# Kernel optimization log

Hardware: AMD Instinct MI355X
Metric: run time of the kernel (lower is better)

Reference implementation:

```python
import jax, jax.numpy as jnp
import numpy as np

B, S, H, W, C = 1, 14, 56, 56, 192
WS = 7            # cubic window
SH = 3            # shift
HEADS = 6
HD = C // HEADS
N = WS ** 3       # 343 tokens per window
NW = (S // WS) * (H // WS) * (W // WS)  # 128 windows
SCALE = HD ** -0.5
HID = 4 * C
TBL = (2 * WS - 1) ** 3  # 2197


def _rel_index():
    # faithful to torch: meshgrid with indexing='xy' and the (3*ws-1)/(2*ws-1) strides
    c = np.stack(np.meshgrid(np.arange(WS), np.arange(WS), np.arange(WS), indexing='xy'))
    f = c.reshape(3, -1)                      # (3, N)
    r = (f[:, :, None] - f[:, None, :]).transpose(1, 2, 0)  # (N, N, 3)
    r = r + (WS - 1)
    r[..., 0] *= 3 * WS - 1
    r[..., 1] *= 2 * WS - 1
    return jnp.asarray(r.sum(-1), dtype=jnp.int32)  # (N, N)

REL_IDX = _rel_index()


def _ln(x, g, b):
    m = x.mean(-1, keepdims=True)
    v = ((x - m) ** 2).mean(-1, keepdims=True)
    return (x - m) * jax.lax.rsqrt(v + 1e-5) * g + b


def _partition(x):  # (B,S,H,W,C) -> (B*nW, N, C)
    x = x.reshape(B, S // WS, WS, H // WS, WS, W // WS, WS, C)
    x = x.transpose(0, 1, 3, 5, 2, 4, 6, 7)
    return x.reshape(-1, N, C)


def _reverse(w):  # (B*nW, N, C) -> (B,S,H,W,C)
    x = w.reshape(B, S // WS, H // WS, W // WS, WS, WS, WS, C)
    x = x.transpose(0, 1, 4, 2, 5, 3, 6, 7)
    return x.reshape(B, S, H, W, C)


def setup_inputs() -> dict:
    key = jax.random.key(0)
    ks = jax.random.split(key, 16)
    L = S * H * W
    p = lambda k, shp, s=0.02: (jax.random.normal(k, shp, dtype=jnp.float32) * s)
    return {
        'x': jax.random.normal(ks[0], (B, L, C), dtype=jnp.float32),
        'mask_matrix': jax.random.normal(ks[1], (NW, N, N), dtype=jnp.float32),
        'skip': jax.random.normal(ks[2], (B, L, C), dtype=jnp.float32),
        'x_up': jax.random.normal(ks[3], (B, L, C), dtype=jnp.float32),
        'norm1_g': jnp.ones((C,), jnp.float32),
        'norm1_b': jnp.zeros((C,), jnp.float32),
        'kv_w': p(ks[4], (C, 2 * C)),
        'kv_b': jnp.zeros((2 * C,), jnp.float32),
        'rel_bias_table': p(ks[5], (TBL, HEADS)),
        'proj_w': p(ks[6], (C, C)),
        'proj_b': jnp.zeros((C,), jnp.float32),
        'norm2_g': jnp.ones((C,), jnp.float32),
        'norm2_b': jnp.zeros((C,), jnp.float32),
        'fc1_w': p(ks[7], (C, HID)),
        'fc1_b': jnp.zeros((HID,), jnp.float32),
        'fc2_w': p(ks[8], (HID, C)),
        'fc2_b': jnp.zeros((C,), jnp.float32),
    }


def reference(x, mask_matrix, skip, x_up, norm1_g, norm1_b, kv_w, kv_b,
              rel_bias_table, proj_w, proj_b, norm2_g, norm2_b,
              fc1_w, fc1_b, fc2_w, fc2_b):
    shortcut = x
    sk = _ln(skip, norm1_g, norm1_b).reshape(B, S, H, W, C)
    xu = _ln(x_up, norm1_g, norm1_b).reshape(B, S, H, W, C)
    # cyclic shift (shift_size > 0, dims divisible by window -> no padding)
    sk = jnp.roll(sk, (-SH, -SH, -SH), axis=(1, 2, 3))
    xu = jnp.roll(xu, (-SH, -SH, -SH), axis=(1, 2, 3))
    sk_w = _partition(sk)   # (Bw, N, C)
    xu_w = _partition(xu)
    Bw = sk_w.shape[0]
    kv = (sk_w @ kv_w + kv_b).reshape(Bw, N, 2, HEADS, HD)
    k = kv[:, :, 0].transpose(0, 2, 1, 3)   # (Bw, h, N, d)
    v = kv[:, :, 1].transpose(0, 2, 1, 3)
    q = xu_w.reshape(Bw, N, HEADS, HD).transpose(0, 2, 1, 3) * SCALE
    attn = jnp.einsum('bhnd,bhmd->bhnm', q, k)
    bias = rel_bias_table[REL_IDX].transpose(2, 0, 1)  # (h, N, N)
    attn = attn + bias[None]
    attn = attn.reshape(B, NW, HEADS, N, N) + mask_matrix[None, :, None]
    attn = jax.nn.softmax(attn.reshape(Bw, HEADS, N, N), axis=-1)
    out = jnp.einsum('bhnm,bhmd->bhnd', attn, v)
    out = out.transpose(0, 2, 1, 3).reshape(Bw, N, C)
    out = out @ proj_w + proj_b
    xr = _reverse(out)
    xr = jnp.roll(xr, (SH, SH, SH), axis=(1, 2, 3)).reshape(B, S * H * W, C)
    x = shortcut + xr
    h = _ln(x, norm2_g, norm2_b)
    h = jax.nn.gelu(h @ fc1_w + fc1_b, approximate=False) @ fc2_w + fc2_b
    return x + h
```

## Files before the change

### kernel.cpp

```cpp
#include <hip/hip_runtime.h>
#include <cstddef>

typedef unsigned short u16;
typedef unsigned int   u32;
typedef __bf16 bf16_t;
typedef bf16_t bf16x8 __attribute__((ext_vector_type(8)));
typedef float  f32x4  __attribute__((ext_vector_type(4)));
typedef u16    u16x4  __attribute__((ext_vector_type(4)));

#define NPAD 352
#define VTS  352
#define PSTR 356

__device__ __forceinline__ u16 f2b(float f) {
  return __builtin_bit_cast(u16, (__bf16)f);
}
__device__ __forceinline__ float b2f(u16 h) {
  return __uint_as_float(((u32)h) << 16);
}
__device__ __forceinline__ f32x4 mfma16(bf16x8 a, bf16x8 b, f32x4 c) {
  return __builtin_amdgcn_mfma_f32_16x16x32_bf16(a, b, c, 0, 0, 0);
}
__device__ __forceinline__ void gl_lds16(const void* g, void* l) {
  __builtin_amdgcn_global_load_lds((const __attribute__((address_space(1))) void*)g,
                                   (__attribute__((address_space(3))) void*)l, 16, 0, 0);
}

__device__ __forceinline__ int win_to_global(int w, int n) {
  int ws = w >> 6, wh = (w >> 3) & 7, ww = w & 7;
  int ts = (n * 1338) >> 16;
  int rem = n - ts * 49;
  int th = (rem * 9363) >> 16;
  int tw = rem - th * 7;
  int gs = ws * 7 + ts + 3; if (gs >= 14) gs -= 14;
  int gh = wh * 7 + th + 3; if (gh >= 56) gh -= 56;
  int gw = ww * 7 + tw + 3; if (gw >= 56) gw -= 56;
  return (gs * 56 + gh) * 56 + gw;
}

__global__ __launch_bounds__(256) void k_wconv(const float* __restrict__ kv_w,
    const float* __restrict__ proj_w, const float* __restrict__ fc1_w,
    const float* __restrict__ fc2_w, u16* kvT, u16* projT, u16* fc1T, u16* fc2T) {
  int t = blockIdx.x * 256 + threadIdx.x;
  if (t < 384 * 192) { int nn = t / 192, kk = t - nn * 192; kvT[t] = f2b(kv_w[kk * 384 + nn]); return; }
  t -= 384 * 192;
  if (t < 256 * 192) { int nn = t / 192, kk = t - nn * 192; projT[t] = (nn < 192) ? f2b(proj_w[kk * 192 + nn]) : (u16)0; return; }
  t -= 256 * 192;
  if (t < 768 * 192) { int nn = t / 192, kk = t - nn * 192; fc1T[t] = f2b(fc1_w[kk * 768 + nn]); return; }
  t -= 768 * 192;
  if (t < 256 * 768) { int nn = t / 768, kk = t - nn * 768; fc2T[t] = (nn < 192) ? f2b(fc2_w[kk * 192 + nn]) : (u16)0; return; }
}

__global__ __launch_bounds__(352) void k_bias(const float* __restrict__ tbl, u16* __restrict__ bf) {
  int m = threadIdx.x, n = blockIdx.x, h = blockIdx.y;
  u16 v = 0;
  if (n < 343 && m < 343) {
    int tsn = (n * 1338) >> 16, remn = n - tsn * 49, thn = (remn * 9363) >> 16, twn = remn - thn * 7;
    int tsm = (m * 1338) >> 16, remm = m - tsm * 49, thm = (remm * 9363) >> 16, twm = remm - thm * 7;
    int idx = (thn - thm) * 20 + (tsn - tsm) * 13 + (twn - twm) + 204;
    v = f2b(tbl[idx * 6 + h]);
  }
  bf[((size_t)h * 352 + n) * 352 + m] = v;
}

__global__ __launch_bounds__(256) void k_maskconv(const float* __restrict__ mask, u16* __restrict__ mb) {
  int t = blockIdx.x * 256 + threadIdx.x;
  int w = t / (352 * 88);
  int r = t - w * (352 * 88);
  int n = r / 88;
  int q = r - n * 88;
  u16x4 v = {0, 0, 0, 0};
  if (n < 343) {
    const float* src = mask + ((size_t)w * 343 + n) * 343 + q * 4;
    #pragma unroll
    for (int j = 0; j < 4; ++j) if (q * 4 + j < 343) v[j] = f2b(src[j]);
  }
  *(u16x4*)&mb[((size_t)w * 352 + n) * 352 + q * 4] = v;
}

__global__ __launch_bounds__(256) void k_ln1(const float* __restrict__ skip, const float* __restrict__ xup,
    const float* __restrict__ g1, const float* __restrict__ b1,
    u16* __restrict__ skw, u16* __restrict__ qb) {
  int wid = threadIdx.x >> 6, lane = threadIdx.x & 63;
  int m = blockIdx.x * 4 + wid;
  u32 w = ((u32)m * 48914u) >> 24;
  int n = m - (int)w * 343;
  int g = win_to_global((int)w, n);
  float xs[3], xu[3];
  float s1 = 0.f, s2 = 0.f, t1 = 0.f, t2 = 0.f;
  #pragma unroll
  for (int i = 0; i < 3; ++i) {
    int c = lane + i * 64;
    xs[i] = skip[(size_t)g * 192 + c];
    xu[i] = xup[(size_t)g * 192 + c];
    s1 += xs[i]; s2 += xs[i] * xs[i];
    t1 += xu[i]; t2 += xu[i] * xu[i];
  }
  #pragma unroll
  for (int off = 1; off < 64; off <<= 1) {
    s1 += __shfl_xor(s1, off); s2 += __shfl_xor(s2, off);
    t1 += __shfl_xor(t1, off); t2 += __shfl_xor(t2, off);
  }
  const float inv = 1.f / 192.f;
  float ms = s1 * inv, vs = s2 * inv - ms * ms;
  float mu = t1 * inv, vu = t2 * inv - mu * mu;
  float rs = rsqrtf(vs + 1e-5f), ru = rsqrtf(vu + 1e-5f);
  #pragma unroll
  for (int i = 0; i < 3; ++i) {
    int c = lane + i * 64;
    float gg = g1[c], bb = b1[c];
    skw[(size_t)m * 192 + c] = f2b((xs[i] - ms) * rs * gg + bb);
    float qv = ((xu[i] - mu) * ru * gg + bb) * 0.17677669529663687f;
    int h = c >> 5, d = c & 31;
    qb[(size_t)(((int)w * 6 + h) * NPAD + n) * 32 + d] = f2b(qv);
  }
}

__global__ __launch_bounds__(256) void k_ln2(const float* __restrict__ xr,
    const float* __restrict__ g2, const float* __restrict__ b2, u16* __restrict__ o) {
  int wid = threadIdx.x >> 6, lane = threadIdx.x & 63;
  int m = blockIdx.x * 4 + wid;
  float v[3]; float s1 = 0.f, s2 = 0.f;
  #pragma unroll
  for (int i = 0; i < 3; ++i) {
    int c = lane + i * 64;
    v[i] = xr[(size_t)m * 192 + c];
    s1 += v[i]; s2 += v[i] * v[i];
  }
  #pragma unroll
  for (int off = 1; off < 64; off <<= 1) { s1 += __shfl_xor(s1, off); s2 += __shfl_xor(s2, off); }
  const float inv = 1.f / 192.f;
  float ms = s1 * inv, vs = s2 * inv - ms * ms;
  float rs = rsqrtf(vs + 1e-5f);
  #pragma unroll
  for (int i = 0; i < 3; ++i) {
    int c = lane + i * 64;
    o[(size_t)m * 192 + c] = f2b((v[i] - ms) * rs * g2[c] + b2[c]);
  }
}

template<int EPI>
__global__ __launch_bounds__(256) void k_gemm(
    const u16* __restrict__ A, const u16* __restrict__ Bm, int K,
    const float* __restrict__ bias,
    u16* __restrict__ outa, u16* __restrict__ outb,
    const float* __restrict__ xin, float* __restrict__ xres,
    float* __restrict__ outf) {
  __shared__ __align__(16) u16 As[128 * 32];
  __shared__ __align__(16) u16 Bs[128 * 32];
  int tid = threadIdx.x;
  int bm = blockIdx.x, bn = blockIdx.y;
  int wid = tid >> 6, lane = tid & 63, lr = lane & 15, lg = lane >> 4;
  int wr = wid >> 1, wc = wid & 1;
  f32x4 acc[4][4] = {};
  const u16* Abase = A + (size_t)bm * 128 * K;
  const u16* Bbase = Bm + (size_t)bn * 128 * K;
  int nk = K >> 5;
  for (int kt = 0; kt < nk; ++kt) {
    int ci0 = tid, ci1 = tid + 256;
    int r0 = ci0 >> 2, c0 = (ci0 & 3) * 8;
    int r1 = ci1 >> 2, c1 = (ci1 & 3) * 8;
    gl_lds16(Abase + (size_t)r0 * K + kt * 32 + c0, &As[ci0 * 8]);
    gl_lds16(Abase + (size_t)r1 * K + kt * 32 + c1, &As[ci1 * 8]);
    gl_lds16(Bbase + (size_t)r0 * K + kt * 32 + c0, &Bs[ci0 * 8]);
    gl_lds16(Bbase + (size_t)r1 * K + kt * 32 + c1, &Bs[ci1 * 8]);
    __syncthreads();
    bf16x8 af[4], bfr[4];
    #pragma unroll
    for (int mi = 0; mi < 4; ++mi) af[mi] = *(const bf16x8*)&As[(wr * 64 + mi * 16 + lr) * 32 + lg * 8];
    #pragma unroll
    for (int ni = 0; ni < 4; ++ni) bfr[ni] = *(const bf16x8*)&Bs[(wc * 64 + ni * 16 + lr) * 32 + lg * 8];
    #pragma unroll
    for (int mi = 0; mi < 4; ++mi)
      #pragma unroll
      for (int ni = 0; ni < 4; ++ni)
        acc[mi][ni] = mfma16(af[mi], bfr[ni], acc[mi][ni]);
    __syncthreads();
  }
  #pragma unroll
  for (int mi = 0; mi < 4; ++mi) {
    #pragma unroll
    for (int r = 0; r < 4; ++r) {
      int grow = bm * 128 + wr * 64 + mi * 16 + lg * 4 + r;
      if (EPI == 0) {
        u32 w = ((u32)grow * 48914u) >> 24; int n = grow - (int)w * 343;
        #pragma unroll
        for (int ni = 0; ni < 4; ++ni) {
          int gcol = bn * 128 + wc * 64 + ni * 16 + lr;
          float v = acc[mi][ni][r] + bias[gcol];
          if (gcol < 192) {
            int hh = gcol >> 5, d = gcol & 31;
            int dswz = ((((d >> 3) ^ ((n >> 1) & 3)) << 3) | (d & 7));
            outa[(size_t)(((int)w * 6 + hh) * NPAD + n) * 32 + dswz] = f2b(v);
          } else {
            int c2 = gcol - 192; int hh = c2 >> 5, d = c2 & 31;
            int nswz = ((((n >> 3) ^ ((d >> 1) & 3)) << 3) | (n & 7));
            outb[(size_t)(((int)w * 6 + hh) * 32 + d) * VTS + nswz] = f2b(v);
          }
        }
      } else if (EPI == 1) {
        u32 w = ((u32)grow * 48914u) >> 24; int n = grow - (int)w * 343;
        int g = win_to_global((int)w, n);
        #pragma unroll
        for (int ni = 0; ni < 4; ++ni) {
          int gcol = bn * 128 + wc * 64 + ni * 16 + lr;
          if (gcol < 192) {
            float v = acc[mi][ni][r] + bias[gcol] + xin[(size_t)g * 192 + gcol];
            xres[(size_t)g * 192 + gcol] = v;
          }
        }
      } else if (EPI == 2) {
        #pragma unroll
        for (int ni = 0; ni < 4; ++ni) {
          int gcol = bn * 128 + wc * 64 + ni * 16 + lr;
          float v = acc[mi][ni][r] + bias[gcol];
          v = 0.5f * v * (1.f + erff(v * 0.7071067811865476f));
          outa[(size_t)grow * 768 + gcol] = f2b(v);
        }
      } else {
        #pragma unroll
        for (int ni = 0; ni < 4; ++ni) {
          int gcol = bn * 128 + wc * 64 + ni * 16 + lr;
          if (gcol < 192)
            outf[(size_t)grow * 192 + gcol] = acc[mi][ni][r] + bias[gcol] + xin[(size_t)grow * 192 + gcol];
        }
      }
    }
  }
}

__global__ __launch_bounds__(256, 1) void k_attn(const u16* __restrict__ qb, const u16* __restrict__ kb,
    const u16* __restrict__ vtb, const u16* __restrict__ bfull, const u16* __restrict__ maskbf,
    u16* __restrict__ att) {
  __shared__ __align__(16) u16 KV[2816 * 8];
  __shared__ __align__(16) u16 P[4][16 * PSTR];
  int bid = blockIdx.x;
  int xcd = bid & 7, i = bid >> 3;
  int wl = i / 6, h = i - wl * 6;
  int w = xcd * 16 + wl;
  int tid = threadIdx.x, wid = tid >> 6, lane = tid & 63, lr = lane & 15, lg = lane >> 4;
  const u16* Q  = qb  + (size_t)(w * 6 + h) * NPAD * 32;
  const u16* Kg = kb  + (size_t)(w * 6 + h) * NPAD * 32;
  const u16* Vg = vtb + (size_t)(w * 6 + h) * 32 * VTS;
  const u16* Bp = bfull + (size_t)h * 352 * 352;
  const u16* Mp = maskbf + (size_t)w * 352 * 352;
  #pragma unroll
  for (int it = 0; it < 11; ++it) {
    int idx = it * 256 + tid;
    if (idx < 1408) gl_lds16(Kg + idx * 8, &KV[idx * 8]);
    else            gl_lds16(Vg + (idx - 1408) * 8, &KV[idx * 8]);
  }
  __syncthreads();
  const u16* Vl = &KV[1408 * 8];
  u16* Pl = &P[wid][0];
  int swz = (lr >> 1) & 3;
  for (int rt = wid; rt < 22; rt += 4) {
    int n = rt * 16 + lr;
    bf16x8 qa = *(const bf16x8*)&Q[(size_t)n * 32 + lg * 8];
    const u16* br = Bp + (size_t)n * 352 + lg * 4;
    const u16* mr = Mp + (size_t)n * 352 + lg * 4;
    u16x4 bb[22], mm[22];
    #pragma unroll
    for (int ct = 0; ct < 22; ++ct) {
      bb[ct] = *(const u16x4*)&br[ct * 16];
      mm[ct] = *(const u16x4*)&mr[ct * 16];
    }
    f32x4 s[22];
    #pragma unroll
    for (int ct = 0; ct < 22; ++ct) {
      bf16x8 kf = *(const bf16x8*)&KV[(ct * 16 + lr) * 32 + (lg ^ swz) * 8];
      f32x4 c;
      #pragma unroll
      for (int r = 0; r < 4; ++r) c[r] = b2f(bb[ct][r]) + b2f(mm[ct][r]);
      s[ct] = mfma16(kf, qa, c);
    }
    { int m0 = 336 + lg * 4;
      #pragma unroll
      for (int r = 0; r < 4; ++r) if (m0 + r >= 343) s[21][r] = -1e30f; }
    float mx = -1e30f;
    #pragma unroll
    for (int ct = 0; ct < 22; ++ct)
      mx = fmaxf(mx, fmaxf(fmaxf(s[ct][0], s[ct][1]), fmaxf(s[ct][2], s[ct][3])));
    mx = fmaxf(mx, __shfl_xor(mx, 16));
    mx = fmaxf(mx, __shfl_xor(mx, 32));
    float t = 0.f;
    #pragma unroll
    for (int ct = 0; ct < 22; ++ct)
      #pragma unroll
      for (int r = 0; r < 4; ++r) { float p = __expf(s[ct][r] - mx); s[ct][r] = p; t += p; }
    t += __shfl_xor(t, 16);
    t += __shfl_xor(t, 32);
    float rs = 1.f / t;
    #pragma unroll
    for (int ct = 0; ct < 22; ++ct) {
      u16x4 pk;
      #pragma unroll
      for (int r = 0; r < 4; ++r) pk[r] = f2b(s[ct][r] * rs);
      *(u16x4*)&Pl[lr * PSTR + ct * 16 + lg * 4] = pk;
    }
    f32x4 o0 = {0.f, 0.f, 0.f, 0.f}, o1 = {0.f, 0.f, 0.f, 0.f};
    #pragma unroll
    for (int ks = 0; ks < 11; ++ks) {
      bf16x8 pa = *(const bf16x8*)&Pl[lr * PSTR + ks * 32 + lg * 8];
      bf16x8 v0 = *(const bf16x8*)&Vl[lr * 352 + ks * 32 + (lg ^ swz) * 8];
      bf16x8 v1 = *(const bf16x8*)&Vl[(16 + lr) * 352 + ks * 32 + (lg ^ swz) * 8];
      o0 = mfma16(pa, v0, o0);
      o1 = mfma16(pa, v1, o1);
    }
    #pragma unroll
    for (int r = 0; r < 4; ++r) {
      Pl[(lg * 4 + r) * 32 + lr] = f2b(o0[r]);
      Pl[(lg * 4 + r) * 32 + 16 + lr] = f2b(o1[r]);
    }
    if (rt * 16 + lr < 343) {
      bf16x8 ov = *(const bf16x8*)&Pl[lr * 32 + lg * 8];
      *(bf16x8*)&att[((size_t)w * 343 + rt * 16 + lr) * 192 + h * 32 + lg * 8] = ov;
    }
  }
}

static const size_t OFF_W    = 0;
static const size_t OFF_XRES = (size_t)1 << 20;
static const size_t OFF_MASK = OFF_XRES;
static const size_t OFF_LN2  = OFF_XRES + ((size_t)34 << 20);
static const size_t OFF_SKW  = OFF_LN2  + ((size_t)17 << 20);
static const size_t OFF_Q    = OFF_SKW  + ((size_t)17 << 20);
static const size_t OFF_K    = OFF_Q    + ((size_t)17 << 20);
static const size_t OFF_VT   = OFF_K    + ((size_t)17 << 20);
static const size_t OFF_ATT  = OFF_VT   + ((size_t)17 << 20);
static const size_t OFF_BIAS = OFF_ATT  + ((size_t)17 << 20);
static const size_t OFF_FC1  = OFF_SKW;

extern "C" void kernel_launch(void* const* d_in, const int* in_sizes, int n_in,
                              void* d_out, int out_size, void* d_ws, size_t ws_size,
                              hipStream_t stream) {
  const float* x      = (const float*)d_in[0];
  const float* mask   = (const float*)d_in[1];
  const float* skip   = (const float*)d_in[2];
  const float* xup    = (const float*)d_in[3];
  const float* n1g    = (const float*)d_in[4];
  const float* n1b    = (const float*)d_in[5];
  const float* kv_w   = (const float*)d_in[6];
  const float* kv_b   = (const float*)d_in[7];
  const float* tbl    = (const float*)d_in[8];
  const float* proj_w = (const float*)d_in[9];
  const float* proj_b = (const float*)d_in[10];
  const float* n2g    = (const float*)d_in[11];
  const float* n2b    = (const float*)d_in[12];
  const float* fc1_w  = (const float*)d_in[13];
  const float* fc1_b  = (const float*)d_in[14];
  const float* fc2_w  = (const float*)d_in[15];
  const float* fc2_b  = (const float*)d_in[16];
  char* ws = (char*)d_ws;
  u16* kvT   = (u16*)(ws + OFF_W);
  u16* projT = kvT + 384 * 192;
  u16* fc1T  = projT + 256 * 192;
  u16* fc2T  = fc1T + 768 * 192;
  float* xres = (float*)(ws + OFF_XRES);
  u16* maskbf = (u16*)(ws + OFF_MASK);
  u16* ln2o  = (u16*)(ws + OFF_LN2);
  u16* skw   = (u16*)(ws + OFF_SKW);
  u16* qb    = (u16*)(ws + OFF_Q);
  u16* kb    = (u16*)(ws + OFF_K);
  u16* vt    = (u16*)(ws + OFF_VT);
  u16* att   = (u16*)(ws + OFF_ATT);
  u16* bfull = (u16*)(ws + OFF_BIAS);
  u16* fc1o  = (u16*)(ws + OFF_FC1);
  float* outp = (float*)d_out;

  k_wconv<<<dim3(1824), dim3(256), 0, stream>>>(kv_w, proj_w, fc1_w, fc2_w, kvT, projT, fc1T, fc2T);
  k_bias<<<dim3(352, 6), dim3(352), 0, stream>>>(tbl, bfull);
  k_maskconv<<<dim3(15488), dim3(256), 0, stream>>>(mask, maskbf);
  k_ln1<<<dim3(10976), dim3(256), 0, stream>>>(skip, xup, n1g, n1b, skw, qb);
  k_gemm<0><<<dim3(343, 3), dim3(256), 0, stream>>>(skw, kvT, 192, kv_b, kb, vt, nullptr, nullptr, nullptr);
  k_attn<<<dim3(768), dim3(256), 0, stream>>>(qb, kb, vt, bfull, maskbf, att);
  k_gemm<1><<<dim3(343, 2), dim3(256), 0, stream>>>(att, projT, 192, proj_b, nullptr, nullptr, x, xres, nullptr);
  k_ln2<<<dim3(10976), dim3(256), 0, stream>>>(xres, n2g, n2b, ln2o);
  k_gemm<2><<<dim3(343, 6), dim3(256), 0, stream>>>(ln2o, fc1T, 192, fc1_b, fc1o, nullptr, nullptr, nullptr, nullptr);
  k_gemm<3><<<dim3(343, 2), dim3(256), 0, stream>>>(fc1o, fc2T, 768, fc2_b, nullptr, nullptr, xres, nullptr, outp);
}
```

Baseline: 353.7 us.

## Read fp32 mask directly in attention, split row tiles, and remap GEMM blocks per XCD

Drops the separate mask-to-bf16 conversion kernel; the attention kernel now reads the fp32 mask rows directly and adds the bias before the QK MFMA. Attention is split into two halves per (window, head), giving twice the blocks, and runs at occupancy 2 with only K staged in LDS, while V is read straight from global memory unswizzled. The window-reverse scatter moves from the proj GEMM epilogue to the attention output store, so the later stages work in global token order. GEMM grids become 1D with an XCD-aware block mapping for L2 locality. Risks are uncoalesced misaligned fp32 mask loads and uncached global V reads inside the inner loop.

```diff
diff --git a/kernel.cpp b/kernel.cpp
--- a/kernel.cpp
+++ b/kernel.cpp
@@ -6,6 +6,7 @@
 typedef __bf16 bf16_t;
 typedef bf16_t bf16x8 __attribute__((ext_vector_type(8)));
 typedef float  f32x4  __attribute__((ext_vector_type(4)));
+typedef float  f32x4u __attribute__((ext_vector_type(4), aligned(4)));
 typedef u16    u16x4  __attribute__((ext_vector_type(4)));
 
 #define NPAD 352
@@ -63,21 +64,6 @@
   bf[((size_t)h * 352 + n) * 352 + m] = v;
 }
 
-__global__ __launch_bounds__(256) void k_maskconv(const float* __restrict__ mask, u16* __restrict__ mb) {
-  int t = blockIdx.x * 256 + threadIdx.x;
-  int w = t / (352 * 88);
-  int r = t - w * (352 * 88);
-  int n = r / 88;
-  int q = r - n * 88;
-  u16x4 v = {0, 0, 0, 0};
-  if (n < 343) {
-    const float* src = mask + ((size_t)w * 343 + n) * 343 + q * 4;
-    #pragma unroll
-    for (int j = 0; j < 4; ++j) if (q * 4 + j < 343) v[j] = f2b(src[j]);
-  }
-  *(u16x4*)&mb[((size_t)w * 352 + n) * 352 + q * 4] = v;
-}
-
 __global__ __launch_bounds__(256) void k_ln1(const float* __restrict__ skip, const float* __restrict__ xup,
     const float* __restrict__ g1, const float* __restrict__ b1,
     u16* __restrict__ skw, u16* __restrict__ qb) {
@@ -141,15 +127,19 @@
 
 template<int EPI>
 __global__ __launch_bounds__(256) void k_gemm(
-    const u16* __restrict__ A, const u16* __restrict__ Bm, int K,
+    const u16* __restrict__ A, const u16* __restrict__ Bm, int K, int nbn,
     const float* __restrict__ bias,
     u16* __restrict__ outa, u16* __restrict__ outb,
     const float* __restrict__ xin, float* __restrict__ xres,
     float* __restrict__ outf) {
   __shared__ __align__(16) u16 As[128 * 32];
   __shared__ __align__(16) u16 Bs[128 * 32];
+  int bid = blockIdx.x;
+  int xcd = bid & 7, j = bid >> 3;
+  int bn = j % nbn, bmL = j / nbn;
+  int bm = xcd * 43 + bmL;
+  if (bm >= 343) return;
   int tid = threadIdx.x;
-  int bm = blockIdx.x, bn = blockIdx.y;
   int wid = tid >> 6, lane = tid & 63, lr = lane & 15, lg = lane >> 4;
   int wr = wid >> 1, wc = wid & 1;
   f32x4 acc[4][4] = {};
@@ -194,19 +184,16 @@
             outa[(size_t)(((int)w * 6 + hh) * NPAD + n) * 32 + dswz] = f2b(v);
           } else {
             int c2 = gcol - 192; int hh = c2 >> 5, d = c2 & 31;
-            int nswz = ((((n >> 3) ^ ((d >> 1) & 3)) << 3) | (n & 7));
-            outb[(size_t)(((int)w * 6 + hh) * 32 + d) * VTS + nswz] = f2b(v);
+            outb[(size_t)(((int)w * 6 + hh) * 32 + d) * VTS + n] = f2b(v);
           }
         }
       } else if (EPI == 1) {
-        u32 w = ((u32)grow * 48914u) >> 24; int n = grow - (int)w * 343;
-        int g = win_to_global((int)w, n);
         #pragma unroll
         for (int ni = 0; ni < 4; ++ni) {
           int gcol = bn * 128 + wc * 64 + ni * 16 + lr;
           if (gcol < 192) {
-            float v = acc[mi][ni][r] + bias[gcol] + xin[(size_t)g * 192 + gcol];
-            xres[(size_t)g * 192 + gcol] = v;
+            float v = acc[mi][ni][r] + bias[gcol] + xin[(size_t)grow * 192 + gcol];
+            xres[(size_t)grow * 192 + gcol] = v;
           }
         }
       } else if (EPI == 2) {
@@ -229,13 +216,14 @@
   }
 }
 
-__global__ __launch_bounds__(256, 1) void k_attn(const u16* __restrict__ qb, const u16* __restrict__ kb,
-    const u16* __restrict__ vtb, const u16* __restrict__ bfull, const u16* __restrict__ maskbf,
+__global__ __launch_bounds__(256, 2) void k_attn(const u16* __restrict__ qb, const u16* __restrict__ kb,
+    const u16* __restrict__ vtb, const u16* __restrict__ bfull, const float* __restrict__ mask,
     u16* __restrict__ att) {
-  __shared__ __align__(16) u16 KV[2816 * 8];
+  __shared__ __align__(16) u16 Ks[1408 * 8];
   __shared__ __align__(16) u16 P[4][16 * PSTR];
   int bid = blockIdx.x;
-  int xcd = bid & 7, i = bid >> 3;
+  int xcd = bid & 7, t = bid >> 3;
+  int half = t & 1, i = t >> 1;
   int wl = i / 6, h = i - wl * 6;
   int w = xcd * 16 + wl;
   int tid = threadIdx.x, wid = tid >> 6, lane = tid & 63, lr = lane & 15, lg = lane >> 4;
@@ -243,36 +231,41 @@
   const u16* Kg = kb  + (size_t)(w * 6 + h) * NPAD * 32;
   const u16* Vg = vtb + (size_t)(w * 6 + h) * 32 * VTS;
   const u16* Bp = bfull + (size_t)h * 352 * 352;
-  const u16* Mp = maskbf + (size_t)w * 352 * 352;
-  #pragma unroll
-  for (int it = 0; it < 11; ++it) {
+  const float* Mp = mask + (size_t)w * 343 * 343;
+  #pragma unroll
+  for (int it = 0; it < 6; ++it) {
     int idx = it * 256 + tid;
-    if (idx < 1408) gl_lds16(Kg + idx * 8, &KV[idx * 8]);
-    else            gl_lds16(Vg + (idx - 1408) * 8, &KV[idx * 8]);
+    if (idx < 1408) gl_lds16(Kg + idx * 8, &Ks[idx * 8]);
   }
   __syncthreads();
-  const u16* Vl = &KV[1408 * 8];
   u16* Pl = &P[wid][0];
   int swz = (lr >> 1) & 3;
-  for (int rt = wid; rt < 22; rt += 4) {
+  int rt_end = half * 11 + 11;
+  for (int rt = half * 11 + wid; rt < rt_end; rt += 4) {
     int n = rt * 16 + lr;
+    int nc = n < 343 ? n : 342;
     bf16x8 qa = *(const bf16x8*)&Q[(size_t)n * 32 + lg * 8];
-    const u16* br = Bp + (size_t)n * 352 + lg * 4;
-    const u16* mr = Mp + (size_t)n * 352 + lg * 4;
-    u16x4 bb[22], mm[22];
+    const float* mrow = Mp + (size_t)nc * 343;
+    const u16* brow = Bp + (size_t)nc * 352;
+    f32x4 s[22];
+    #pragma unroll
+    for (int ct = 0; ct < 21; ++ct) {
+      int m0 = ct * 16 + lg * 4;
+      f32x4u mm = *(const f32x4u*)&mrow[m0];
+      u16x4 bb = *(const u16x4*)&brow[m0];
+      #pragma unroll
+      for (int r = 0; r < 4; ++r) s[ct][r] = mm[r] + b2f(bb[r]);
+    }
+    {
+      int m0 = 336 + lg * 4;
+      #pragma unroll
+      for (int r = 0; r < 4; ++r)
+        s[21][r] = (m0 + r < 343) ? (mrow[m0 + r] + b2f(brow[m0 + r])) : 0.f;
+    }
     #pragma unroll
     for (int ct = 0; ct < 22; ++ct) {
-      bb[ct] = *(const u16x4*)&br[ct * 16];
-      mm[ct] = *(const u16x4*)&mr[ct * 16];
-    }
-    f32x4 s[22];
-    #pragma unroll
-    for (int ct = 0; ct < 22; ++ct) {
-      bf16x8 kf = *(const bf16x8*)&KV[(ct * 16 + lr) * 32 + (lg ^ swz) * 8];
-      f32x4 c;
-      #pragma unroll
-      for (int r = 0; r < 4; ++r) c[r] = b2f(bb[ct][r]) + b2f(mm[ct][r]);
-      s[ct] = mfma16(kf, qa, c);
+      bf16x8 kf = *(const bf16x8*)&Ks[(ct * 16 + lr) * 32 + (lg ^ swz) * 8];
+      s[ct] = mfma16(kf, qa, s[ct]);
     }
     { int m0 = 336 + lg * 4;
       #pragma unroll
@@ -283,14 +276,14 @@
       mx = fmaxf(mx, fmaxf(fmaxf(s[ct][0], s[ct][1]), fmaxf(s[ct][2], s[ct][3])));
     mx = fmaxf(mx, __shfl_xor(mx, 16));
     mx = fmaxf(mx, __shfl_xor(mx, 32));
-    float t = 0.f;
+    float tsum = 0.f;
     #pragma unroll
     for (int ct = 0; ct < 22; ++ct)
       #pragma unroll
-      for (int r = 0; r < 4; ++r) { float p = __expf(s[ct][r] - mx); s[ct][r] = p; t += p; }
-    t += __shfl_xor(t, 16);
-    t += __shfl_xor(t, 32);
-    float rs = 1.f / t;
+      for (int r = 0; r < 4; ++r) { float p = __expf(s[ct][r] - mx); s[ct][r] = p; tsum += p; }
+    tsum += __shfl_xor(tsum, 16);
+    tsum += __shfl_xor(tsum, 32);
+    float rs = 1.f / tsum;
     #pragma unroll
     for (int ct = 0; ct < 22; ++ct) {
       u16x4 pk;
@@ -302,8 +295,8 @@
     #pragma unroll
     for (int ks = 0; ks < 11; ++ks) {
       bf16x8 pa = *(const bf16x8*)&Pl[lr * PSTR + ks * 32 + lg * 8];
-      bf16x8 v0 = *(const bf16x8*)&Vl[lr * 352 + ks * 32 + (lg ^ swz) * 8];
-      bf16x8 v1 = *(const bf16x8*)&Vl[(16 + lr) * 352 + ks * 32 + (lg ^ swz) * 8];
+      bf16x8 v0 = *(const bf16x8*)&Vg[(size_t)lr * VTS + ks * 32 + lg * 8];
+      bf16x8 v1 = *(const bf16x8*)&Vg[(size_t)(16 + lr) * VTS + ks * 32 + lg * 8];
       o0 = mfma16(pa, v0, o0);
       o1 = mfma16(pa, v1, o1);
     }
@@ -312,16 +305,16 @@
       Pl[(lg * 4 + r) * 32 + lr] = f2b(o0[r]);
       Pl[(lg * 4 + r) * 32 + 16 + lr] = f2b(o1[r]);
     }
-    if (rt * 16 + lr < 343) {
+    if (n < 343) {
+      int g = win_to_global(w, n);
       bf16x8 ov = *(const bf16x8*)&Pl[lr * 32 + lg * 8];
-      *(bf16x8*)&att[((size_t)w * 343 + rt * 16 + lr) * 192 + h * 32 + lg * 8] = ov;
+      *(bf16x8*)&att[(size_t)g * 192 + h * 32 + lg * 8] = ov;
     }
   }
 }
 
 static const size_t OFF_W    = 0;
 static const size_t OFF_XRES = (size_t)1 << 20;
-static const size_t OFF_MASK = OFF_XRES;
 static const size_t OFF_LN2  = OFF_XRES + ((size_t)34 << 20);
 static const size_t OFF_SKW  = OFF_LN2  + ((size_t)17 << 20);
 static const size_t OFF_Q    = OFF_SKW  + ((size_t)17 << 20);
@@ -357,7 +350,6 @@
   u16* fc1T  = projT + 256 * 192;
   u16* fc2T  = fc1T + 768 * 192;
   float* xres = (float*)(ws + OFF_XRES);
-  u16* maskbf = (u16*)(ws + OFF_MASK);
   u16* ln2o  = (u16*)(ws + OFF_LN2);
   u16* skw   = (u16*)(ws + OFF_SKW);
   u16* qb    = (u16*)(ws + OFF_Q);
@@ -370,12 +362,11 @@
 
   k_wconv<<<dim3(1824), dim3(256), 0, stream>>>(kv_w, proj_w, fc1_w, fc2_w, kvT, projT, fc1T, fc2T);
   k_bias<<<dim3(352, 6), dim3(352), 0, stream>>>(tbl, bfull);
-  k_maskconv<<<dim3(15488), dim3(256), 0, stream>>>(mask, maskbf);
   k_ln1<<<dim3(10976), dim3(256), 0, stream>>>(skip, xup, n1g, n1b, skw, qb);
-  k_gemm<0><<<dim3(343, 3), dim3(256), 0, stream>>>(skw, kvT, 192, kv_b, kb, vt, nullptr, nullptr, nullptr);
-  k_attn<<<dim3(768), dim3(256), 0, stream>>>(qb, kb, vt, bfull, maskbf, att);
-  k_gemm<1><<<dim3(343, 2), dim3(256), 0, stream>>>(att, projT, 192, proj_b, nullptr, nullptr, x, xres, nullptr);
+  k_gemm<0><<<dim3(8 * 43 * 3), dim3(256), 0, stream>>>(skw, kvT, 192, 3, kv_b, kb, vt, nullptr, nullptr, nullptr);
+  k_attn<<<dim3(1536), dim3(256), 0, stream>>>(qb, kb, vt, bfull, mask, att);
+  k_gemm<1><<<dim3(8 * 43 * 2), dim3(256), 0, stream>>>(att, projT, 192, 2, proj_b, nullptr, nullptr, x, xres, nullptr);
   k_ln2<<<dim3(10976), dim3(256), 0, stream>>>(xres, n2g, n2b, ln2o);
-  k_gemm<2><<<dim3(343, 6), dim3(256), 0, stream>>>(ln2o, fc1T, 192, fc1_b, fc1o, nullptr, nullptr, nullptr, nullptr);
-  k_gemm<3><<<dim3(343, 2), dim3(256), 0, stream>>>(fc1o, fc2T, 768, fc2_b, nullptr, nullptr, xres, nullptr, outp);
-}
+  k_gemm<2><<<dim3(8 * 43 * 6), dim3(256), 0, stream>>>(ln2o, fc1T, 192, 6, fc1_b, fc1o, nullptr, nullptr, nullptr, nullptr);
+  k_gemm<3><<<dim3(8 * 43 * 2), dim3(256), 0, stream>>>(fc1o, fc2T, 768, 2, fc2_b, nullptr, nullptr, xres, nullptr, outp);
+}
```

Result: slower. 379.4 us (+7.3%).
